# Performance work log

Measured on AMD Instinct MI355X. Metric: run time of the kernel, lower is better.

Reference implementation:

```python
import jax, jax.numpy as jnp
import numpy as np
from jax import lax

N_ITER = 5   # self.n from __init__
K = 2.0      # self.k from __init__

def _avg_pool2(x):
    B, C, H, W = x.shape
    return x.reshape(B, C, H // 2, 2, W // 2, 2).mean(axis=(3, 5))

def _max_pool2(x):
    B, C, H, W = x.shape
    return x.reshape(B, C, H // 2, 2, W // 2, 2).max(axis=(3, 5))

def _box_dilate(x):
    # 3x3 all-ones conv, stride 1, padding 1, single channel
    k = jnp.ones((1, 1, 3, 3), x.dtype)
    return lax.conv_general_dilated(x, k, (1, 1), ((1, 1), (1, 1)),
                                    dimension_numbers=('NCHW', 'OIHW', 'NCHW'))

def setup_inputs() -> dict:
    key = jax.random.key(0)
    k1, k2, k3, k4, k5, k6, k7 = jax.random.split(key, 7)
    B, Cf, Hf, Wf = 8, 256, 128, 128
    H, W = 512, 512
    F_in = jax.random.normal(k1, (B, Cf, Hf, Wf), jnp.float32)
    img_p = jax.random.uniform(k2, (B, 3, H, W), jnp.float32)
    m = jax.random.randint(k3, (B, 1, H, W), 0, 2).astype(jnp.float32)
    mask = jnp.tile(m, (1, 3, 1, 1))
    gamma_w = jax.random.normal(k4, (Cf, 3), jnp.float32) * 0.1
    gamma_b = jax.random.normal(k5, (Cf,), jnp.float32) * 0.1
    beta_w = jax.random.normal(k6, (Cf, 3), jnp.float32) * 0.1
    beta_b = jax.random.normal(k7, (Cf,), jnp.float32) * 0.1
    return {"F_in": F_in, "img_p": img_p, "mask": mask,
            "gamma_w": gamma_w, "gamma_b": gamma_b,
            "beta_w": beta_w, "beta_b": beta_b,
            "n_ds": 2, "n": 2}

def reference(F_in, img_p, mask, gamma_w, gamma_b, beta_w, beta_b, n_ds, n):
    for _ in range(n_ds):
        img_p = _avg_pool2(img_p)
        mask = _max_pool2(mask)
    mask = mask[:, :1]                         # torch.chunk(..., 3)[0]
    D_h = mask
    msk = (mask == 1.0)
    for i in range(1, N_ITER + 1):
        D_h = _box_dilate(D_h)
        tmp = (D_h > 0) & (~msk)               # newly reached pixels
        msk = msk | tmp
        mask = jnp.where(tmp, 1.0 / K ** i, mask)
        D_h = mask
    gamma_hp = jnp.einsum('bchw,oc->bohw', img_p, gamma_w) + gamma_b[None, :, None, None]
    beta_hp = jnp.einsum('bchw,oc->bohw', img_p, beta_w) + beta_b[None, :, None, None]
    if n == 1:
        gamma_hd = lax.stop_gradient(gamma_hp) * D_h
        beta_hd = lax.stop_gradient(beta_hp) * D_h
    else:
        gamma_hd = gamma_hp * D_h
        beta_hd = beta_hp * D_h
    mean = jnp.mean(F_in)
    var = jnp.var(F_in, ddof=1)                # torch.var default unbiased
    F_norm = (F_in - mean) / jnp.sqrt(var ** 2 + 1e-5)  # var**2 as in source
    return F_norm * gamma_hd + beta_hd
```

## Files before the change

### kernel.cpp

```cpp
#include <hip/hip_runtime.h>
#include <math.h>

constexpr int B  = 8;
constexpr int CF = 256;
constexpr int HF = 128;
constexpr int WF = 128;
constexpr int HP = 512;
constexpr int WP = 512;
constexpr long long NTOT = (long long)B * CF * HF * WF;

constexpr size_t STATS_OFF = 0;
constexpr size_t DH_OFF    = 256;
constexpr size_t IMG_OFF   = DH_OFF + (size_t)B * HF * WF * sizeof(float);

constexpr int RBLOCKS  = 1024;
constexpr int RTHREADS = 256;

__global__ void __launch_bounds__(RTHREADS) k_reduce(const float* __restrict__ F,
                                                     double2* __restrict__ part) {
    const long long tid = (long long)blockIdx.x * RTHREADS + threadIdx.x;
    const long long S  = (long long)RBLOCKS * RTHREADS * 4;
    double s0 = 0, s1 = 0, s2 = 0, s3 = 0;
    double q0 = 0, q1 = 0, q2 = 0, q3 = 0;
    for (long long base = tid * 4; base < NTOT; base += 8 * S) {
        float4 v0 = *(const float4*)(F + base + 0 * S);
        float4 v1 = *(const float4*)(F + base + 1 * S);
        float4 v2 = *(const float4*)(F + base + 2 * S);
        float4 v3 = *(const float4*)(F + base + 3 * S);
        float4 v4 = *(const float4*)(F + base + 4 * S);
        float4 v5 = *(const float4*)(F + base + 5 * S);
        float4 v6 = *(const float4*)(F + base + 6 * S);
        float4 v7 = *(const float4*)(F + base + 7 * S);
        s0 += (double)v0.x + (double)v0.y + (double)v0.z + (double)v0.w;
        q0 += (double)v0.x * v0.x + (double)v0.y * v0.y + (double)v0.z * v0.z + (double)v0.w * v0.w;
        s1 += (double)v1.x + (double)v1.y + (double)v1.z + (double)v1.w;
        q1 += (double)v1.x * v1.x + (double)v1.y * v1.y + (double)v1.z * v1.z + (double)v1.w * v1.w;
        s2 += (double)v2.x + (double)v2.y + (double)v2.z + (double)v2.w;
        q2 += (double)v2.x * v2.x + (double)v2.y * v2.y + (double)v2.z * v2.z + (double)v2.w * v2.w;
        s3 += (double)v3.x + (double)v3.y + (double)v3.z + (double)v3.w;
        q3 += (double)v3.x * v3.x + (double)v3.y * v3.y + (double)v3.z * v3.z + (double)v3.w * v3.w;
        s0 += (double)v4.x + (double)v4.y + (double)v4.z + (double)v4.w;
        q0 += (double)v4.x * v4.x + (double)v4.y * v4.y + (double)v4.z * v4.z + (double)v4.w * v4.w;
        s1 += (double)v5.x + (double)v5.y + (double)v5.z + (double)v5.w;
        q1 += (double)v5.x * v5.x + (double)v5.y * v5.y + (double)v5.z * v5.z + (double)v5.w * v5.w;
        s2 += (double)v6.x + (double)v6.y + (double)v6.z + (double)v6.w;
        q2 += (double)v6.x * v6.x + (double)v6.y * v6.y + (double)v6.z * v6.z + (double)v6.w * v6.w;
        s3 += (double)v7.x + (double)v7.y + (double)v7.z + (double)v7.w;
        q3 += (double)v7.x * v7.x + (double)v7.y * v7.y + (double)v7.z * v7.z + (double)v7.w * v7.w;
    }
    double s = (s0 + s1) + (s2 + s3);
    double q = (q0 + q1) + (q2 + q3);
    for (int off = 32; off > 0; off >>= 1) {
        s += __shfl_down(s, off);
        q += __shfl_down(q, off);
    }
    __shared__ double ls[4], lq[4];
    int lane = threadIdx.x & 63, wv = threadIdx.x >> 6;
    if (lane == 0) { ls[wv] = s; lq[wv] = q; }
    __syncthreads();
    if (threadIdx.x == 0) {
        double S_ = 0.0, Q_ = 0.0;
        for (int w = 0; w < 4; ++w) { S_ += ls[w]; Q_ += lq[w]; }
        part[blockIdx.x] = make_double2(S_, Q_);
    }
}

__global__ void k_stats(const double2* __restrict__ part, float* __restrict__ stats) {
    double s = 0.0, q = 0.0;
    for (int i = threadIdx.x; i < RBLOCKS; i += 256) {
        double2 p = part[i];
        s += p.x; q += p.y;
    }
    for (int off = 32; off > 0; off >>= 1) {
        s += __shfl_down(s, off);
        q += __shfl_down(q, off);
    }
    __shared__ double ls[4], lq[4];
    int lane = threadIdx.x & 63, wv = threadIdx.x >> 6;
    if (lane == 0) { ls[wv] = s; lq[wv] = q; }
    __syncthreads();
    if (threadIdx.x == 0) {
        double S_ = 0.0, Q_ = 0.0;
        for (int w = 0; w < 4; ++w) { S_ += ls[w]; Q_ += lq[w]; }
        double mean = S_ / (double)NTOT;
        double var  = (Q_ - (double)NTOT * mean * mean) / (double)(NTOT - 1);
        stats[0] = (float)mean;
        stats[1] = (float)(1.0 / sqrt(var * var + 1e-5));
    }
}

__global__ void k_pool(const float* __restrict__ img, const float* __restrict__ mask,
                       float* __restrict__ img_ds, float* __restrict__ mds) {
    int t = blockIdx.x * blockDim.x + threadIdx.x;
    if (t >= B * HF * WF) return;
    int w = t & (WF - 1);
    int h = (t >> 7) & (HF - 1);
    int b = t >> 14;
    for (int c = 0; c < 3; ++c) {
        const float* p = img + (((b * 3 + c) * HP + h * 4) * WP + w * 4);
        float s = 0.0f;
        for (int r = 0; r < 4; ++r) {
            float4 v = *(const float4*)(p + r * WP);
            s += v.x + v.y + v.z + v.w;
        }
        img_ds[(((b * 3 + c)) << 14) | (h << 7) | w] = s * 0.0625f;
    }
    const float* pm = mask + (((b * 3) * HP + h * 4) * WP + w * 4);
    float m = 0.0f;
    for (int r = 0; r < 4; ++r) {
        float4 v = *(const float4*)(pm + r * WP);
        m = fmaxf(m, fmaxf(fmaxf(v.x, v.y), fmaxf(v.z, v.w)));
    }
    mds[t] = m;
}

__global__ void __launch_bounds__(1024) k_dilate(const float* __restrict__ mds,
                                                 float* __restrict__ Dh) {
    __shared__ float M[HF * WF];
    const int b = blockIdx.x;
    const float* src = mds + b * HF * WF;
    for (int i = threadIdx.x; i < HF * WF; i += 1024) M[i] = src[i];
    __syncthreads();
    float invk = 1.0f;
    for (int it = 1; it <= 5; ++it) {
        invk *= 0.5f;
        unsigned nf = 0;
        for (int j = 0; j < 16; ++j) {
            int p = threadIdx.x + j * 1024;
            if (M[p] != 0.0f) continue;
            int h = p >> 7, w = p & 127;
            bool any = false;
            for (int dh = -1; dh <= 1; ++dh) {
                int hh = h + dh;
                if (hh < 0 || hh >= HF) continue;
                for (int dw = -1; dw <= 1; ++dw) {
                    int ww = w + dw;
                    if (ww < 0 || ww >= WF) continue;
                    any = any || (M[(hh << 7) | ww] > 0.0f);
                }
            }
            if (any) nf |= (1u << j);
        }
        __syncthreads();
        for (int j = 0; j < 16; ++j)
            if (nf & (1u << j)) M[threadIdx.x + j * 1024] = invk;
        __syncthreads();
    }
    float* dst = Dh + b * HF * WF;
    for (int i = threadIdx.x; i < HF * WF; i += 1024) dst[i] = M[i];
}

__global__ void k_final(const float* __restrict__ F,
                        const float* __restrict__ img_ds,
                        const float* __restrict__ Dh,
                        const float* __restrict__ gw, const float* __restrict__ gb,
                        const float* __restrict__ bw, const float* __restrict__ bb,
                        const float* __restrict__ stats,
                        float* __restrict__ out) {
    long long t = (long long)blockIdx.x * blockDim.x + threadIdx.x;
    long long base = t * 4;
    if (base >= NTOT) return;
    int w = (int)(base & 127);
    int h = (int)((base >> 7) & 127);
    int c = (int)((base >> 14) & 255);
    int b = (int)(base >> 22);

    float meanf = stats[0];
    float rstd  = stats[1];

    int pix = (b << 14) | (h << 7) | w;
    float4 D = *(const float4*)(Dh + pix);
    const float* ip = img_ds + ((size_t)b * 3 << 14);
    float4 R  = *(const float4*)(ip + ((0 << 14) | (h << 7) | w));
    float4 G  = *(const float4*)(ip + ((1 << 14) | (h << 7) | w));
    float4 Bl = *(const float4*)(ip + ((2 << 14) | (h << 7) | w));

    float g0 = gw[c * 3], g1 = gw[c * 3 + 1], g2 = gw[c * 3 + 2], gbi = gb[c];
    float b0 = bw[c * 3], b1 = bw[c * 3 + 1], b2 = bw[c * 3 + 2], bbi = bb[c];

    float4 Fv = *(const float4*)(F + base);
    float4 o;
    {
        float gam = (R.x * g0 + G.x * g1 + Bl.x * g2 + gbi) * D.x;
        float bet = (R.x * b0 + G.x * b1 + Bl.x * b2 + bbi) * D.x;
        o.x = (Fv.x - meanf) * rstd * gam + bet;
    }
    {
        float gam = (R.y * g0 + G.y * g1 + Bl.y * g2 + gbi) * D.y;
        float bet = (R.y * b0 + G.y * b1 + Bl.y * b2 + bbi) * D.y;
        o.y = (Fv.y - meanf) * rstd * gam + bet;
    }
    {
        float gam = (R.z * g0 + G.z * g1 + Bl.z * g2 + gbi) * D.z;
        float bet = (R.z * b0 + G.z * b1 + Bl.z * b2 + bbi) * D.z;
        o.z = (Fv.z - meanf) * rstd * gam + bet;
    }
    {
        float gam = (R.w * g0 + G.w * g1 + Bl.w * g2 + gbi) * D.w;
        float bet = (R.w * b0 + G.w * b1 + Bl.w * b2 + bbi) * D.w;
        o.w = (Fv.w - meanf) * rstd * gam + bet;
    }
    *(float4*)(out + base) = o;
}

extern "C" void kernel_launch(void* const* d_in, const int* in_sizes, int n_in,
                              void* d_out, int out_size, void* d_ws, size_t ws_size,
                              hipStream_t stream) {
    const float* F_in  = (const float*)d_in[0];
    const float* img_p = (const float*)d_in[1];
    const float* mask  = (const float*)d_in[2];
    const float* gw    = (const float*)d_in[3];
    const float* gb    = (const float*)d_in[4];
    const float* bw    = (const float*)d_in[5];
    const float* bb    = (const float*)d_in[6];
    float* out = (float*)d_out;

    float*   stats  = (float*)((char*)d_ws + STATS_OFF);
    float*   Dh     = (float*)((char*)d_ws + DH_OFF);
    float*   img_ds = (float*)((char*)d_ws + IMG_OFF);
    double2* part   = (double2*)img_ds;

    k_reduce<<<RBLOCKS, RTHREADS, 0, stream>>>(F_in, part);
    k_stats<<<1, 256, 0, stream>>>(part, stats);
    k_pool<<<(B * HF * WF + 255) / 256, 256, 0, stream>>>(img_p, mask, img_ds, Dh);
    k_dilate<<<B, 1024, 0, stream>>>(Dh, Dh);
    k_final<<<(int)((NTOT / 4 + 255) / 256), 256, 0, stream>>>(
        F_in, img_ds, Dh, gw, gb, bw, bb, stats, out);
}
```

Baseline: 310.2 us.

## Restructure reduction, fold stats into dilate, channel-group final kernel with nontemporal IO

```diff
diff --git a/kernel.cpp b/kernel.cpp
--- a/kernel.cpp
+++ b/kernel.cpp
@@ -9,44 +9,49 @@
 constexpr int WP = 512;
 constexpr long long NTOT = (long long)B * CF * HF * WF;
 
+typedef float f4 __attribute__((ext_vector_type(4)));
+
 constexpr size_t STATS_OFF = 0;
 constexpr size_t DH_OFF    = 256;
 constexpr size_t IMG_OFF   = DH_OFF + (size_t)B * HF * WF * sizeof(float);
-
-constexpr int RBLOCKS  = 1024;
+constexpr size_t PART_OFF  = IMG_OFF + (size_t)B * 3 * HF * WF * sizeof(float);
+
+constexpr int RBLOCKS  = 2048;
 constexpr int RTHREADS = 256;
+constexpr long long CH_S = (long long)RBLOCKS * RTHREADS * 4;
 
 __global__ void __launch_bounds__(RTHREADS) k_reduce(const float* __restrict__ F,
                                                      double2* __restrict__ part) {
     const long long tid = (long long)blockIdx.x * RTHREADS + threadIdx.x;
-    const long long S  = (long long)RBLOCKS * RTHREADS * 4;
+    const float* p = F + tid * 4;
+    f4 v[16];
+#pragma unroll
+    for (int k = 0; k < 16; ++k)
+        v[k] = *(const f4*)(p + k * CH_S);
     double s0 = 0, s1 = 0, s2 = 0, s3 = 0;
     double q0 = 0, q1 = 0, q2 = 0, q3 = 0;
-    for (long long base = tid * 4; base < NTOT; base += 8 * S) {
-        float4 v0 = *(const float4*)(F + base + 0 * S);
-        float4 v1 = *(const float4*)(F + base + 1 * S);
-        float4 v2 = *(const float4*)(F + base + 2 * S);
-        float4 v3 = *(const float4*)(F + base + 3 * S);
-        float4 v4 = *(const float4*)(F + base + 4 * S);
-        float4 v5 = *(const float4*)(F + base + 5 * S);
-        float4 v6 = *(const float4*)(F + base + 6 * S);
-        float4 v7 = *(const float4*)(F + base + 7 * S);
-        s0 += (double)v0.x + (double)v0.y + (double)v0.z + (double)v0.w;
-        q0 += (double)v0.x * v0.x + (double)v0.y * v0.y + (double)v0.z * v0.z + (double)v0.w * v0.w;
-        s1 += (double)v1.x + (double)v1.y + (double)v1.z + (double)v1.w;
-        q1 += (double)v1.x * v1.x + (double)v1.y * v1.y + (double)v1.z * v1.z + (double)v1.w * v1.w;
-        s2 += (double)v2.x + (double)v2.y + (double)v2.z + (double)v2.w;
-        q2 += (double)v2.x * v2.x + (double)v2.y * v2.y + (double)v2.z * v2.z + (double)v2.w * v2.w;
-        s3 += (double)v3.x + (double)v3.y + (double)v3.z + (double)v3.w;
-        q3 += (double)v3.x * v3.x + (double)v3.y * v3.y + (double)v3.z * v3.z + (double)v3.w * v3.w;
-        s0 += (double)v4.x + (double)v4.y + (double)v4.z + (double)v4.w;
-        q0 += (double)v4.x * v4.x + (double)v4.y * v4.y + (double)v4.z * v4.z + (double)v4.w * v4.w;
-        s1 += (double)v5.x + (double)v5.y + (double)v5.z + (double)v5.w;
-        q1 += (double)v5.x * v5.x + (double)v5.y * v5.y + (double)v5.z * v5.z + (double)v5.w * v5.w;
-        s2 += (double)v6.x + (double)v6.y + (double)v6.z + (double)v6.w;
-        q2 += (double)v6.x * v6.x + (double)v6.y * v6.y + (double)v6.z * v6.z + (double)v6.w * v6.w;
-        s3 += (double)v7.x + (double)v7.y + (double)v7.z + (double)v7.w;
-        q3 += (double)v7.x * v7.x + (double)v7.y * v7.y + (double)v7.z * v7.z + (double)v7.w * v7.w;
+#pragma unroll
+    for (int k = 0; k < 16; k += 4) {
+        {
+            f4 w = v[k + 0];
+            s0 += (double)((w.x + w.y) + (w.z + w.w));
+            q0 += (double)((w.x * w.x + w.y * w.y) + (w.z * w.z + w.w * w.w));
+        }
+        {
+            f4 w = v[k + 1];
+            s1 += (double)((w.x + w.y) + (w.z + w.w));
+            q1 += (double)((w.x * w.x + w.y * w.y) + (w.z * w.z + w.w * w.w));
+        }
+        {
+            f4 w = v[k + 2];
+            s2 += (double)((w.x + w.y) + (w.z + w.w));
+            q2 += (double)((w.x * w.x + w.y * w.y) + (w.z * w.z + w.w * w.w));
+        }
+        {
+            f4 w = v[k + 3];
+            s3 += (double)((w.x + w.y) + (w.z + w.w));
+            q3 += (double)((w.x * w.x + w.y * w.y) + (w.z * w.z + w.w * w.w));
+        }
     }
     double s = (s0 + s1) + (s2 + s3);
     double q = (q0 + q1) + (q2 + q3);
@@ -62,30 +67,6 @@
         double S_ = 0.0, Q_ = 0.0;
         for (int w = 0; w < 4; ++w) { S_ += ls[w]; Q_ += lq[w]; }
         part[blockIdx.x] = make_double2(S_, Q_);
-    }
-}
-
-__global__ void k_stats(const double2* __restrict__ part, float* __restrict__ stats) {
-    double s = 0.0, q = 0.0;
-    for (int i = threadIdx.x; i < RBLOCKS; i += 256) {
-        double2 p = part[i];
-        s += p.x; q += p.y;
-    }
-    for (int off = 32; off > 0; off >>= 1) {
-        s += __shfl_down(s, off);
-        q += __shfl_down(q, off);
-    }
-    __shared__ double ls[4], lq[4];
-    int lane = threadIdx.x & 63, wv = threadIdx.x >> 6;
-    if (lane == 0) { ls[wv] = s; lq[wv] = q; }
-    __syncthreads();
-    if (threadIdx.x == 0) {
-        double S_ = 0.0, Q_ = 0.0;
-        for (int w = 0; w < 4; ++w) { S_ += ls[w]; Q_ += lq[w]; }
-        double mean = S_ / (double)NTOT;
-        double var  = (Q_ - (double)NTOT * mean * mean) / (double)(NTOT - 1);
-        stats[0] = (float)mean;
-        stats[1] = (float)(1.0 / sqrt(var * var + 1e-5));
     }
 }
 
@@ -100,7 +81,7 @@
         const float* p = img + (((b * 3 + c) * HP + h * 4) * WP + w * 4);
         float s = 0.0f;
         for (int r = 0; r < 4; ++r) {
-            float4 v = *(const float4*)(p + r * WP);
+            f4 v = *(const f4*)(p + r * WP);
             s += v.x + v.y + v.z + v.w;
         }
         img_ds[(((b * 3 + c)) << 14) | (h << 7) | w] = s * 0.0625f;
@@ -108,18 +89,43 @@
     const float* pm = mask + (((b * 3) * HP + h * 4) * WP + w * 4);
     float m = 0.0f;
     for (int r = 0; r < 4; ++r) {
-        float4 v = *(const float4*)(pm + r * WP);
+        f4 v = *(const f4*)(pm + r * WP);
         m = fmaxf(m, fmaxf(fmaxf(v.x, v.y), fmaxf(v.z, v.w)));
     }
     mds[t] = m;
 }
 
-__global__ void __launch_bounds__(1024) k_dilate(const float* __restrict__ mds,
-                                                 float* __restrict__ Dh) {
+__global__ void __launch_bounds__(1024) k_dilate_stats(float* __restrict__ Dh,
+                                                       const double2* __restrict__ part,
+                                                       float* __restrict__ stats) {
+    if (blockIdx.x == 8) {
+        double s = 0.0, q = 0.0;
+        for (int i = threadIdx.x; i < RBLOCKS; i += 1024) {
+            double2 p = part[i];
+            s += p.x; q += p.y;
+        }
+        for (int off = 32; off > 0; off >>= 1) {
+            s += __shfl_down(s, off);
+            q += __shfl_down(q, off);
+        }
+        __shared__ double ls[16], lq[16];
+        int lane = threadIdx.x & 63, wv = threadIdx.x >> 6;
+        if (lane == 0) { ls[wv] = s; lq[wv] = q; }
+        __syncthreads();
+        if (threadIdx.x == 0) {
+            double S_ = 0.0, Q_ = 0.0;
+            for (int w = 0; w < 16; ++w) { S_ += ls[w]; Q_ += lq[w]; }
+            double mean = S_ / (double)NTOT;
+            double var  = (Q_ - (double)NTOT * mean * mean) / (double)(NTOT - 1);
+            stats[0] = (float)mean;
+            stats[1] = (float)(1.0 / sqrt(var * var + 1e-5));
+        }
+        return;
+    }
     __shared__ float M[HF * WF];
     const int b = blockIdx.x;
-    const float* src = mds + b * HF * WF;
-    for (int i = threadIdx.x; i < HF * WF; i += 1024) M[i] = src[i];
+    float* img = Dh + b * HF * WF;
+    for (int i = threadIdx.x; i < HF * WF; i += 1024) M[i] = img[i];
     __syncthreads();
     float invk = 1.0f;
     for (int it = 1; it <= 5; ++it) {
@@ -146,61 +152,71 @@
             if (nf & (1u << j)) M[threadIdx.x + j * 1024] = invk;
         __syncthreads();
     }
-    float* dst = Dh + b * HF * WF;
-    for (int i = threadIdx.x; i < HF * WF; i += 1024) dst[i] = M[i];
-}
-
-__global__ void k_final(const float* __restrict__ F,
+    for (int i = threadIdx.x; i < HF * WF; i += 1024) img[i] = M[i];
+}
+
+constexpr int CGRP = 8;
+__global__ void __launch_bounds__(256) k_final(const float* __restrict__ F,
                         const float* __restrict__ img_ds,
                         const float* __restrict__ Dh,
                         const float* __restrict__ gw, const float* __restrict__ gb,
                         const float* __restrict__ bw, const float* __restrict__ bb,
                         const float* __restrict__ stats,
                         float* __restrict__ out) {
-    long long t = (long long)blockIdx.x * blockDim.x + threadIdx.x;
-    long long base = t * 4;
-    if (base >= NTOT) return;
-    int w = (int)(base & 127);
-    int h = (int)((base >> 7) & 127);
-    int c = (int)((base >> 14) & 255);
-    int b = (int)(base >> 22);
+    long long tid = (long long)blockIdx.x * blockDim.x + threadIdx.x;
+    int iw  = (int)(tid & 31);
+    int ih  = (int)((tid >> 5) & 127);
+    int icg = (int)((tid >> 12) & 31);
+    int ib  = (int)(tid >> 17);
+    int w   = iw * 4;
+    int c0  = icg * CGRP;
 
     float meanf = stats[0];
     float rstd  = stats[1];
 
-    int pix = (b << 14) | (h << 7) | w;
-    float4 D = *(const float4*)(Dh + pix);
-    const float* ip = img_ds + ((size_t)b * 3 << 14);
-    float4 R  = *(const float4*)(ip + ((0 << 14) | (h << 7) | w));
-    float4 G  = *(const float4*)(ip + ((1 << 14) | (h << 7) | w));
-    float4 Bl = *(const float4*)(ip + ((2 << 14) | (h << 7) | w));
-
-    float g0 = gw[c * 3], g1 = gw[c * 3 + 1], g2 = gw[c * 3 + 2], gbi = gb[c];
-    float b0 = bw[c * 3], b1 = bw[c * 3 + 1], b2 = bw[c * 3 + 2], bbi = bb[c];
-
-    float4 Fv = *(const float4*)(F + base);
-    float4 o;
-    {
-        float gam = (R.x * g0 + G.x * g1 + Bl.x * g2 + gbi) * D.x;
-        float bet = (R.x * b0 + G.x * b1 + Bl.x * b2 + bbi) * D.x;
-        o.x = (Fv.x - meanf) * rstd * gam + bet;
-    }
-    {
-        float gam = (R.y * g0 + G.y * g1 + Bl.y * g2 + gbi) * D.y;
-        float bet = (R.y * b0 + G.y * b1 + Bl.y * b2 + bbi) * D.y;
-        o.y = (Fv.y - meanf) * rstd * gam + bet;
-    }
-    {
-        float gam = (R.z * g0 + G.z * g1 + Bl.z * g2 + gbi) * D.z;
-        float bet = (R.z * b0 + G.z * b1 + Bl.z * b2 + bbi) * D.z;
-        o.z = (Fv.z - meanf) * rstd * gam + bet;
-    }
-    {
-        float gam = (R.w * g0 + G.w * g1 + Bl.w * g2 + gbi) * D.w;
-        float bet = (R.w * b0 + G.w * b1 + Bl.w * b2 + bbi) * D.w;
-        o.w = (Fv.w - meanf) * rstd * gam + bet;
-    }
-    *(float4*)(out + base) = o;
+    int pixoff = (ih << 7) | w;
+    int pix = (ib << 14) | pixoff;
+    f4 D = *(const f4*)(Dh + pix);
+    const float* ip = img_ds + ((size_t)ib * 3 << 14);
+    f4 R  = *(const f4*)(ip + ((0 << 14) | pixoff));
+    f4 G  = *(const f4*)(ip + ((1 << 14) | pixoff));
+    f4 Bl = *(const f4*)(ip + ((2 << 14) | pixoff));
+
+    const size_t fbase = (((size_t)(ib * CF + c0)) << 14) + pixoff;
+
+    f4 Fv[CGRP];
+#pragma unroll
+    for (int j = 0; j < CGRP; ++j)
+        Fv[j] = __builtin_nontemporal_load((const f4*)(F + fbase + ((size_t)j << 14)));
+
+#pragma unroll
+    for (int j = 0; j < CGRP; ++j) {
+        int c = c0 + j;
+        float g0 = gw[c * 3], g1 = gw[c * 3 + 1], g2 = gw[c * 3 + 2], gbi = gb[c];
+        float b0 = bw[c * 3], b1 = bw[c * 3 + 1], b2 = bw[c * 3 + 2], bbi = bb[c];
+        f4 o;
+        {
+            float gam = (R.x * g0 + G.x * g1 + Bl.x * g2 + gbi) * D.x;
+            float bet = (R.x * b0 + G.x * b1 + Bl.x * b2 + bbi) * D.x;
+            o.x = (Fv[j].x - meanf) * rstd * gam + bet;
+        }
+        {
+            float gam = (R.y * g0 + G.y * g1 + Bl.y * g2 + gbi) * D.y;
+            float bet = (R.y * b0 + G.y * b1 + Bl.y * b2 + bbi) * D.y;
+            o.y = (Fv[j].y - meanf) * rstd * gam + bet;
+        }
+        {
+            float gam = (R.z * g0 + G.z * g1 + Bl.z * g2 + gbi) * D.z;
+            float bet = (R.z * b0 + G.z * b1 + Bl.z * b2 + bbi) * D.z;
+            o.z = (Fv[j].z - meanf) * rstd * gam + bet;
+        }
+        {
+            float gam = (R.w * g0 + G.w * g1 + Bl.w * g2 + gbi) * D.w;
+            float bet = (R.w * b0 + G.w * b1 + Bl.w * b2 + bbi) * D.w;
+            o.w = (Fv[j].w - meanf) * rstd * gam + bet;
+        }
+        __builtin_nontemporal_store(o, (f4*)(out + fbase + ((size_t)j << 14)));
+    }
 }
 
 extern "C" void kernel_launch(void* const* d_in, const int* in_sizes, int n_in,
@@ -218,12 +234,11 @@
     float*   stats  = (float*)((char*)d_ws + STATS_OFF);
     float*   Dh     = (float*)((char*)d_ws + DH_OFF);
     float*   img_ds = (float*)((char*)d_ws + IMG_OFF);
-    double2* part   = (double2*)img_ds;
+    double2* part   = (double2*)((char*)d_ws + PART_OFF);
 
     k_reduce<<<RBLOCKS, RTHREADS, 0, stream>>>(F_in, part);
-    k_stats<<<1, 256, 0, stream>>>(part, stats);
     k_pool<<<(B * HF * WF + 255) / 256, 256, 0, stream>>>(img_p, mask, img_ds, Dh);
-    k_dilate<<<B, 1024, 0, stream>>>(Dh, Dh);
-    k_final<<<(int)((NTOT / 4 + 255) / 256), 256, 0, stream>>>(
+    k_dilate_stats<<<B + 1, 1024, 0, stream>>>(Dh, part, stats);
+    k_final<<<(int)(NTOT / (4 * CGRP) / 256), 256, 0, stream>>>(
         F_in, img_ds, Dh, gw, gb, bw, bb, stats, out);
 }
```

Measured after the change: 305.9 us. No clear change (-1.4%).
